# Kernel tuning notes

Measured on AMD Instinct MI355X. Metric: run time of the kernel, lower is better.

The kernel has to match this reference:

```python
import jax, jax.numpy as jnp
import numpy as np

N = 32768   # atoms/nodes
E = 4       # chemical elements
C = 128     # input channels per irrep
K = 128     # output channels per irrep
LMAX = 3    # 4 l-blocks -> 16 lm rows


def setup_inputs() -> dict:
    key = jax.random.key(0)
    kx, ky, kw = jax.random.split(key, 3)
    x = jax.random.normal(kx, (N, (LMAX + 1) ** 2, C), dtype=jnp.float32)
    # one-hot element encoding per node
    elem = jax.random.randint(ky, (N,), 0, E)
    y = jax.nn.one_hot(elem, E, dtype=jnp.float32)
    # per-element, per-l weight blocks [E, 4, C, K]
    weights = jax.random.normal(kw, (E, LMAX + 1, C, K), dtype=jnp.float32)
    return {"x": x, "y": y, "weights": weights}


def reference(x, y, weights):
    # x: [N, 16, C]  y: [N, E] one-hot  weights: [E, 4, C, K]
    n, _, c = x.shape
    e, nl, _, k = weights.shape
    path_weight = 1.0 / jnp.sqrt(jnp.asarray(c, x.dtype))  # e3nn uvw normalization
    outs = []
    for l in range(nl):
        s = l * l
        m = 2 * l + 1
        xb = x[:, s:s + m, :]                      # [N, 2l+1, C]
        acc = jnp.zeros((n, m, k), x.dtype)
        for el in range(e):
            # mask-weighted grouped GEMM: only nodes of element `el` contribute
            acc = acc + y[:, el, None, None] * jnp.einsum('nmc,ck->nmk', xb, weights[el, l])
        outs.append(acc * path_weight)
    return jnp.concatenate(outs, axis=1)           # [N, 16, K]
```

## Files before the change

kernel.cpp:

```cpp
#include <hip/hip_runtime.h>

#define NS 32768
#define NE 4

typedef __attribute__((ext_vector_type(4))) float f32x4;
typedef __attribute__((ext_vector_type(8))) short bf16x8;

__device__ __forceinline__ unsigned short f2bf(float f) {
    unsigned int u = __float_as_uint(f);
    u = (u + 0x7fffu + ((u >> 16) & 1u)) >> 16;
    return (unsigned short)u;
}

__device__ __forceinline__ int expert_of(const float4 yr) {
    int e = 0;
    if (yr.y > 0.5f) e = 1;
    else if (yr.z > 0.5f) e = 2;
    else if (yr.w > 0.5f) e = 3;
    return e;
}

__global__ void prep_count(const float* __restrict__ W,
                           unsigned short* __restrict__ Wt,
                           const float* __restrict__ y,
                           int* __restrict__ bcnt) {
    const int b = blockIdx.x;
    if (b < 16) {
        const float* w = W + (size_t)b * 16384;
        unsigned short* wt = Wt + (size_t)b * 16384;
        for (int i = threadIdx.x; i < 16384; i += 256) {
            int c = i & 127, k = i >> 7;
            wt[k * 128 + c] = f2bf(w[c * 128 + k]);
        }
        return;
    }
    const int blk = b - 16;
    int n = blk * 256 + threadIdx.x;
    int e = expert_of(((const float4*)y)[n]);
    const int lane = threadIdx.x & 63;
#pragma unroll
    for (int ee = 0; ee < NE; ++ee) {
        unsigned long long m = __ballot(e == ee);
        if (lane == 0 && m) atomicAdd(&bcnt[ee * 128 + blk], __popcll(m));
    }
}

__global__ void prep_scan(const int* __restrict__ bcnt, int* __restrict__ boff,
                          int* __restrict__ cnt) {
    __shared__ int s[512];
    const int t = threadIdx.x;
    int v = bcnt[t];
    s[t] = v;
    __syncthreads();
    for (int d = 1; d < 512; d <<= 1) {
        int add = (t >= d) ? s[t - d] : 0;
        __syncthreads();
        s[t] += add;
        __syncthreads();
    }
    int seg = (t >= 128) ? s[(t >> 7) * 128 - 1] : 0;
    boff[t] = s[t] - v - seg;
    if ((t & 127) == 127) cnt[t >> 7] = s[t] - seg;
}

__global__ void prep_fill(const float* __restrict__ y,
                          const int* __restrict__ boff, int* __restrict__ idx) {
    __shared__ int wcnt[4][4];
    const int blk = blockIdx.x;
    int n = blk * 256 + threadIdx.x;
    int e = expert_of(((const float4*)y)[n]);
    const int lane = threadIdx.x & 63;
    const int wv = threadIdx.x >> 6;
    int rank = 0;
#pragma unroll
    for (int ee = 0; ee < NE; ++ee) {
        unsigned long long m = __ballot(e == ee);
        if (lane == 0) wcnt[wv][ee] = __popcll(m);
        if (e == ee) rank = __popcll(m & ((1ull << lane) - 1ull));
    }
    __syncthreads();
#pragma unroll
    for (int w = 0; w < 4; ++w)
        if (w < wv) rank += wcnt[w][e];
    idx[e * NS + boff[e * 128 + blk] + rank] = n;
}

template <int L, int M>
__device__ __forceinline__ void gemm_body(
    int e, int bi, int nb, unsigned char* lds, const float* __restrict__ x,
    const unsigned short* __restrict__ Wt, const int* __restrict__ cnt,
    const int* __restrict__ idx, float* __restrict__ out) {
    const int rows_total = cnt[e] * M;

    {
        const unsigned char* wp =
            (const unsigned char*)(Wt + (size_t)(e * 4 + L) * 16384);
        const int t = threadIdx.x;
#pragma unroll
        for (int q = 0; q < 8; ++q) {
            int o = q * 4096 + t * 16;
            uint4 v = *(const uint4*)(wp + o);
            int so = o ^ (((o >> 8) & 7) << 4);
            *(uint4*)(lds + so) = v;
        }
    }
    __syncthreads();

    const int lane = threadIdx.x & 63;
    const int wv = threadIdx.x >> 6;
    const int li = lane & 15;
    const int half = lane >> 4;
    const int i5 = lane >> 5;
    const int c32 = lane & 31;
    unsigned char* xl = lds + 32768 + wv * 4096;

    for (int tile = bi; tile * 64 < rows_total; tile += nb) {
        int g = tile * 64 + wv * 16 + li;
        bool valid = g < rows_total;
        int gc = valid ? g : rows_total - 1;
        int pos = gc / M;
        int jj = gc - pos * M;
        int xrow = idx[e * NS + pos] * 16 + L * L + jj;

        f32x4 bv[8];
#pragma unroll
        for (int q = 0; q < 8; ++q) {
            int tr = 2 * q + i5;
            int nr = __shfl(xrow, tr);
            bv[q] = *(const f32x4*)(x + (size_t)nr * 128 + c32 * 4);
        }
#pragma unroll
        for (int q = 0; q < 8; ++q) {
            int tr = 2 * q + i5;
            unsigned int p0 = (unsigned int)f2bf(bv[q].x) |
                              ((unsigned int)f2bf(bv[q].y) << 16);
            unsigned int p1 = (unsigned int)f2bf(bv[q].z) |
                              ((unsigned int)f2bf(bv[q].w) << 16);
            uint2 pk; pk.x = p0; pk.y = p1;
            int off = (c32 * 8) ^ ((tr & 7) << 4);
            *(uint2*)(xl + tr * 256 + off) = pk;
        }

        f32x4 acc[8];
#pragma unroll
        for (int t = 0; t < 8; ++t) acc[t] = (f32x4){0.f, 0.f, 0.f, 0.f};

#pragma unroll
        for (int kk = 0; kk < 4; ++kk) {
            int co = (kk * 64 + half * 16) ^ ((li & 7) << 4);
            bf16x8 bfrag = *(const bf16x8*)(xl + li * 256 + co);
#pragma unroll
            for (int t = 0; t < 8; ++t) {
                bf16x8 afrag = *(const bf16x8*)(lds + (t * 16 + li) * 256 + co);
                acc[t] = __builtin_amdgcn_mfma_f32_16x16x32_bf16(afrag, bfrag,
                                                                 acc[t], 0, 0, 0);
            }
        }

        if (valid) {
            float* orow = out + (size_t)xrow * 128;
            const float pw = 0.088388347648318447f;
#pragma unroll
            for (int t = 0; t < 8; ++t) {
                *(f32x4*)(orow + t * 16 + half * 4) = acc[t] * pw;
            }
        }
    }
}

__global__ __launch_bounds__(256, 3) void gemm_main(
    const float* __restrict__ x, const unsigned short* __restrict__ Wt,
    const int* __restrict__ cnt, const int* __restrict__ idx,
    float* __restrict__ out) {
    __shared__ __align__(16) unsigned char lds[49152];
    const int b = blockIdx.x;
    const int e = b >> 9;
    const int r = b & 511;
    if (r < 32)       gemm_body<0, 1>(e, r,       32,  lds, x, Wt, cnt, idx, out);
    else if (r < 128) gemm_body<1, 3>(e, r - 32,  96,  lds, x, Wt, cnt, idx, out);
    else if (r < 288) gemm_body<2, 5>(e, r - 128, 160, lds, x, Wt, cnt, idx, out);
    else              gemm_body<3, 7>(e, r - 288, 224, lds, x, Wt, cnt, idx, out);
}

extern "C" void kernel_launch(void* const* d_in, const int* in_sizes, int n_in,
                              void* d_out, int out_size, void* d_ws,
                              size_t ws_size, hipStream_t stream) {
    const float* x = (const float*)d_in[0];
    const float* y = (const float*)d_in[1];
    const float* W = (const float*)d_in[2];
    float* out = (float*)d_out;

    char* ws = (char*)d_ws;
    int* cnt = (int*)ws;
    int* idx = (int*)(ws + 64);
    unsigned short* Wt = (unsigned short*)(ws + 64 + NE * NS * 4);
    int* bcnt = (int*)(ws + 64 + NE * NS * 4 + 16 * 16384 * 2);
    int* boff = bcnt + 512;

    hipMemsetAsync(bcnt, 0, 512 * sizeof(int), stream);
    prep_count<<<16 + 128, 256, 0, stream>>>(W, Wt, y, bcnt);
    prep_scan<<<1, 512, 0, stream>>>(bcnt, boff, cnt);
    prep_fill<<<128, 256, 0, stream>>>(y, boff, idx);
    gemm_main<<<2048, 256, 0, stream>>>(x, Wt, cnt, idx, out);
}
```

Baseline: 142.6 us.

## Load activation fragments directly into registers, drop LDS staging and memset

The gemm kernel now has each lane load its own 8 consecutive fp32 values per k-step straight from global memory and convert them to a bf16 MFMA B-fragment in registers, removing the LDS write/read round trip for activations. This shrinks LDS to 32 KB, and the launch bound is raised to 4 blocks per CU. prep_count now reduces per-wave counts in shared memory and writes per-block counts directly, which removes the atomics and the separate hipMemsetAsync launch. The trade-off is that each lane now issues 32-byte strided global reads instead of the previous coalesced row loads, and register pressure rises under the tighter occupancy bound.

```diff
diff --git a/kernel.cpp b/kernel.cpp
--- a/kernel.cpp
+++ b/kernel.cpp
@@ -34,15 +34,21 @@
         }
         return;
     }
+    __shared__ int c[4][4];
     const int blk = b - 16;
     int n = blk * 256 + threadIdx.x;
     int e = expert_of(((const float4*)y)[n]);
     const int lane = threadIdx.x & 63;
+    const int wv = threadIdx.x >> 6;
 #pragma unroll
     for (int ee = 0; ee < NE; ++ee) {
         unsigned long long m = __ballot(e == ee);
-        if (lane == 0 && m) atomicAdd(&bcnt[ee * 128 + blk], __popcll(m));
-    }
+        if (lane == 0) c[wv][ee] = __popcll(m);
+    }
+    __syncthreads();
+    if (threadIdx.x < 4)
+        bcnt[threadIdx.x * 128 + blk] = c[0][threadIdx.x] + c[1][threadIdx.x] +
+                                        c[2][threadIdx.x] + c[3][threadIdx.x];
 }
 
 __global__ void prep_scan(const int* __restrict__ bcnt, int* __restrict__ boff,
@@ -110,9 +116,6 @@
     const int wv = threadIdx.x >> 6;
     const int li = lane & 15;
     const int half = lane >> 4;
-    const int i5 = lane >> 5;
-    const int c32 = lane & 31;
-    unsigned char* xl = lds + 32768 + wv * 4096;
 
     for (int tile = bi; tile * 64 < rows_total; tile += nb) {
         int g = tile * 64 + wv * 16 + li;
@@ -122,23 +125,24 @@
         int jj = gc - pos * M;
         int xrow = idx[e * NS + pos] * 16 + L * L + jj;
 
-        f32x4 bv[8];
-#pragma unroll
-        for (int q = 0; q < 8; ++q) {
-            int tr = 2 * q + i5;
-            int nr = __shfl(xrow, tr);
-            bv[q] = *(const f32x4*)(x + (size_t)nr * 128 + c32 * 4);
-        }
-#pragma unroll
-        for (int q = 0; q < 8; ++q) {
-            int tr = 2 * q + i5;
-            unsigned int p0 = (unsigned int)f2bf(bv[q].x) |
-                              ((unsigned int)f2bf(bv[q].y) << 16);
-            unsigned int p1 = (unsigned int)f2bf(bv[q].z) |
-                              ((unsigned int)f2bf(bv[q].w) << 16);
-            uint2 pk; pk.x = p0; pk.y = p1;
-            int off = (c32 * 8) ^ ((tr & 7) << 4);
-            *(uint2*)(xl + tr * 256 + off) = pk;
+        const float* xr = x + (size_t)xrow * 128 + half * 8;
+        f32x4 v0[4], v1[4];
+#pragma unroll
+        for (int kk = 0; kk < 4; ++kk) {
+            v0[kk] = *(const f32x4*)(xr + kk * 32);
+            v1[kk] = *(const f32x4*)(xr + kk * 32 + 4);
+        }
+        bf16x8 bfrag[4];
+#pragma unroll
+        for (int kk = 0; kk < 4; ++kk) {
+            bfrag[kk][0] = (short)f2bf(v0[kk].x);
+            bfrag[kk][1] = (short)f2bf(v0[kk].y);
+            bfrag[kk][2] = (short)f2bf(v0[kk].z);
+            bfrag[kk][3] = (short)f2bf(v0[kk].w);
+            bfrag[kk][4] = (short)f2bf(v1[kk].x);
+            bfrag[kk][5] = (short)f2bf(v1[kk].y);
+            bfrag[kk][6] = (short)f2bf(v1[kk].z);
+            bfrag[kk][7] = (short)f2bf(v1[kk].w);
         }
 
         f32x4 acc[8];
@@ -148,11 +152,10 @@
 #pragma unroll
         for (int kk = 0; kk < 4; ++kk) {
             int co = (kk * 64 + half * 16) ^ ((li & 7) << 4);
-            bf16x8 bfrag = *(const bf16x8*)(xl + li * 256 + co);
 #pragma unroll
             for (int t = 0; t < 8; ++t) {
                 bf16x8 afrag = *(const bf16x8*)(lds + (t * 16 + li) * 256 + co);
-                acc[t] = __builtin_amdgcn_mfma_f32_16x16x32_bf16(afrag, bfrag,
+                acc[t] = __builtin_amdgcn_mfma_f32_16x16x32_bf16(afrag, bfrag[kk],
                                                                  acc[t], 0, 0, 0);
             }
         }
@@ -168,11 +171,11 @@
     }
 }
 
-__global__ __launch_bounds__(256, 3) void gemm_main(
+__global__ __launch_bounds__(256, 4) void gemm_main(
     const float* __restrict__ x, const unsigned short* __restrict__ Wt,
     const int* __restrict__ cnt, const int* __restrict__ idx,
     float* __restrict__ out) {
-    __shared__ __align__(16) unsigned char lds[49152];
+    __shared__ __align__(16) unsigned char lds[32768];
     const int b = blockIdx.x;
     const int e = b >> 9;
     const int r = b & 511;
@@ -197,7 +200,6 @@
     int* bcnt = (int*)(ws + 64 + NE * NS * 4 + 16 * 16384 * 2);
     int* boff = bcnt + 512;
 
-    hipMemsetAsync(bcnt, 0, 512 * sizeof(int), stream);
     prep_count<<<16 + 128, 256, 0, stream>>>(W, Wt, y, bcnt);
     prep_scan<<<1, 512, 0, stream>>>(bcnt, boff, cnt);
     prep_fill<<<128, 256, 0, stream>>>(y, boff, idx);
```

Result: slower. 247.1 us (+73.2%).

## Double-buffer gathered x rows in registers and drop memset with LDS block counts

Applied to the files above, without the earlier changes.

The GEMM tile loop now prefetches the next tile's gathered x rows into a second register buffer while the current tile is converted to bf16 and multiplied. The goal is to hide global gather latency behind MFMA work. Separately, prep_count now reduces per-wave ballot counts in LDS and writes each block count directly, which removes the memset launch and the atomics. The extra 8 f32x4 registers raise register pressure, which may lower occupancy under the 3-block launch bound. In the final iteration a redundant reload of the current tile is issued.

```diff
diff --git a/kernel.cpp b/kernel.cpp
--- a/kernel.cpp
+++ b/kernel.cpp
@@ -34,15 +34,21 @@
         }
         return;
     }
+    __shared__ int c[4][4];
     const int blk = b - 16;
     int n = blk * 256 + threadIdx.x;
     int e = expert_of(((const float4*)y)[n]);
     const int lane = threadIdx.x & 63;
+    const int wv = threadIdx.x >> 6;
 #pragma unroll
     for (int ee = 0; ee < NE; ++ee) {
         unsigned long long m = __ballot(e == ee);
-        if (lane == 0 && m) atomicAdd(&bcnt[ee * 128 + blk], __popcll(m));
-    }
+        if (lane == 0) c[wv][ee] = __popcll(m);
+    }
+    __syncthreads();
+    if (threadIdx.x < 4)
+        bcnt[threadIdx.x * 128 + blk] = c[0][threadIdx.x] + c[1][threadIdx.x] +
+                                        c[2][threadIdx.x] + c[3][threadIdx.x];
 }
 
 __global__ void prep_scan(const int* __restrict__ bcnt, int* __restrict__ boff,
@@ -86,11 +92,72 @@
 }
 
 template <int L, int M>
+__device__ __forceinline__ void load_tile(
+    const float* __restrict__ x, const int* __restrict__ idx, int e,
+    int rows_total, int tile, int wv, int li, int i5, int c32,
+    int& xrow, bool& valid, f32x4* bv) {
+    int g = tile * 64 + wv * 16 + li;
+    valid = g < rows_total;
+    int gc = valid ? g : rows_total - 1;
+    int pos = gc / M;
+    int jj = gc - pos * M;
+    xrow = idx[e * NS + pos] * 16 + L * L + jj;
+#pragma unroll
+    for (int q = 0; q < 8; ++q) {
+        int nr = __shfl(xrow, 2 * q + i5);
+        bv[q] = *(const f32x4*)(x + (size_t)nr * 128 + c32 * 4);
+    }
+}
+
+__device__ __forceinline__ void compute_tile(
+    const unsigned char* __restrict__ lds, unsigned char* __restrict__ xl,
+    const f32x4* bv, int xrow, bool valid, int li, int half, int i5, int c32,
+    float* __restrict__ out) {
+#pragma unroll
+    for (int q = 0; q < 8; ++q) {
+        int tr = 2 * q + i5;
+        unsigned int p0 = (unsigned int)f2bf(bv[q].x) |
+                          ((unsigned int)f2bf(bv[q].y) << 16);
+        unsigned int p1 = (unsigned int)f2bf(bv[q].z) |
+                          ((unsigned int)f2bf(bv[q].w) << 16);
+        uint2 pk; pk.x = p0; pk.y = p1;
+        int off = (c32 * 8) ^ ((tr & 7) << 4);
+        *(uint2*)(xl + tr * 256 + off) = pk;
+    }
+
+    f32x4 acc[8];
+#pragma unroll
+    for (int t = 0; t < 8; ++t) acc[t] = (f32x4){0.f, 0.f, 0.f, 0.f};
+
+#pragma unroll
+    for (int kk = 0; kk < 4; ++kk) {
+        int co = (kk * 64 + half * 16) ^ ((li & 7) << 4);
+        bf16x8 bfrag = *(const bf16x8*)(xl + li * 256 + co);
+#pragma unroll
+        for (int t = 0; t < 8; ++t) {
+            bf16x8 afrag = *(const bf16x8*)(lds + (t * 16 + li) * 256 + co);
+            acc[t] = __builtin_amdgcn_mfma_f32_16x16x32_bf16(afrag, bfrag,
+                                                             acc[t], 0, 0, 0);
+        }
+    }
+
+    if (valid) {
+        float* orow = out + (size_t)xrow * 128;
+        const float pw = 0.088388347648318447f;
+#pragma unroll
+        for (int t = 0; t < 8; ++t) {
+            *(f32x4*)(orow + t * 16 + half * 4) = acc[t] * pw;
+        }
+    }
+}
+
+template <int L, int M>
 __device__ __forceinline__ void gemm_body(
     int e, int bi, int nb, unsigned char* lds, const float* __restrict__ x,
     const unsigned short* __restrict__ Wt, const int* __restrict__ cnt,
     const int* __restrict__ idx, float* __restrict__ out) {
     const int rows_total = cnt[e] * M;
+    const int nt = (rows_total + 63) >> 6;
 
     {
         const unsigned char* wp =
@@ -114,57 +181,28 @@
     const int c32 = lane & 31;
     unsigned char* xl = lds + 32768 + wv * 4096;
 
-    for (int tile = bi; tile * 64 < rows_total; tile += nb) {
-        int g = tile * 64 + wv * 16 + li;
-        bool valid = g < rows_total;
-        int gc = valid ? g : rows_total - 1;
-        int pos = gc / M;
-        int jj = gc - pos * M;
-        int xrow = idx[e * NS + pos] * 16 + L * L + jj;
-
-        f32x4 bv[8];
-#pragma unroll
-        for (int q = 0; q < 8; ++q) {
-            int tr = 2 * q + i5;
-            int nr = __shfl(xrow, tr);
-            bv[q] = *(const f32x4*)(x + (size_t)nr * 128 + c32 * 4);
-        }
-#pragma unroll
-        for (int q = 0; q < 8; ++q) {
-            int tr = 2 * q + i5;
-            unsigned int p0 = (unsigned int)f2bf(bv[q].x) |
-                              ((unsigned int)f2bf(bv[q].y) << 16);
-            unsigned int p1 = (unsigned int)f2bf(bv[q].z) |
-                              ((unsigned int)f2bf(bv[q].w) << 16);
-            uint2 pk; pk.x = p0; pk.y = p1;
-            int off = (c32 * 8) ^ ((tr & 7) << 4);
-            *(uint2*)(xl + tr * 256 + off) = pk;
-        }
-
-        f32x4 acc[8];
-#pragma unroll
-        for (int t = 0; t < 8; ++t) acc[t] = (f32x4){0.f, 0.f, 0.f, 0.f};
-
-#pragma unroll
-        for (int kk = 0; kk < 4; ++kk) {
-            int co = (kk * 64 + half * 16) ^ ((li & 7) << 4);
-            bf16x8 bfrag = *(const bf16x8*)(xl + li * 256 + co);
-#pragma unroll
-            for (int t = 0; t < 8; ++t) {
-                bf16x8 afrag = *(const bf16x8*)(lds + (t * 16 + li) * 256 + co);
-                acc[t] = __builtin_amdgcn_mfma_f32_16x16x32_bf16(afrag, bfrag,
-                                                                 acc[t], 0, 0, 0);
-            }
-        }
-
-        if (valid) {
-            float* orow = out + (size_t)xrow * 128;
-            const float pw = 0.088388347648318447f;
-#pragma unroll
-            for (int t = 0; t < 8; ++t) {
-                *(f32x4*)(orow + t * 16 + half * 4) = acc[t] * pw;
-            }
-        }
+    int tA = bi;
+    if (tA >= nt) return;
+
+    int xrowA, xrowB;
+    bool vA, vB;
+    f32x4 bvA[8], bvB[8];
+
+    load_tile<L, M>(x, idx, e, rows_total, tA, wv, li, i5, c32, xrowA, vA, bvA);
+    for (;;) {
+        int tB = tA + nb;
+        bool hB = tB < nt;
+        load_tile<L, M>(x, idx, e, rows_total, hB ? tB : tA, wv, li, i5, c32,
+                        xrowB, vB, bvB);
+        compute_tile(lds, xl, bvA, xrowA, vA, li, half, i5, c32, out);
+        if (!hB) break;
+        int tC = tB + nb;
+        bool hC = tC < nt;
+        load_tile<L, M>(x, idx, e, rows_total, hC ? tC : tB, wv, li, i5, c32,
+                        xrowA, vA, bvA);
+        compute_tile(lds, xl, bvB, xrowB, vB, li, half, i5, c32, out);
+        if (!hC) break;
+        tA = tC;
     }
 }
 
@@ -197,7 +235,6 @@
     int* bcnt = (int*)(ws + 64 + NE * NS * 4 + 16 * 16384 * 2);
     int* boff = bcnt + 512;
 
-    hipMemsetAsync(bcnt, 0, 512 * sizeof(int), stream);
     prep_count<<<16 + 128, 256, 0, stream>>>(W, Wt, y, bcnt);
     prep_scan<<<1, 512, 0, stream>>>(bcnt, boff, cnt);
     prep_fill<<<128, 256, 0, stream>>>(y, boff, idx);
```

Result: slower. 239.2 us (+67.7%).
